# Optimization experiments

Measured on AMD Instinct MI355X. Metric: run time of the kernel, lower is better.

The kernel has to match this reference:

```python
import jax, jax.numpy as jnp
import numpy as np

B, L, E, H = 2, 2048, 1024, 16
D = E // H


def setup_inputs() -> dict:
    key = jax.random.key(0)
    ks = jax.random.split(key, 6)
    s = 1.0 / np.sqrt(E)
    return {
        "X": jax.random.normal(ks[0], (B, L, E), dtype=jnp.float32),
        "ke_bias": jax.random.normal(ks[1], (B * H, L, L), dtype=jnp.float32) * 0.05,
        "in_proj_w": jax.random.normal(ks[2], (3 * E, E), dtype=jnp.float32) * s,
        "in_proj_b": jnp.zeros((3 * E,), dtype=jnp.float32),
        "out_proj_w": jax.random.normal(ks[3], (E, E), dtype=jnp.float32) * s,
        "out_proj_b": jnp.zeros((E,), dtype=jnp.float32),
    }


def reference(X, ke_bias, in_proj_w, in_proj_b, out_proj_w, out_proj_b):
    # Packed QKV projection, matching nn.MultiheadAttention layout.
    qkv = X @ in_proj_w.T + in_proj_b  # [B, L, 3E]
    q, k, v = jnp.split(qkv, 3, axis=-1)
    # [B, L, E] -> [B, H, L, D]
    q = q.reshape(B, L, H, D).transpose(0, 2, 1, 3)
    k = k.reshape(B, L, H, D).transpose(0, 2, 1, 3)
    v = v.reshape(B, L, H, D).transpose(0, 2, 1, 3)
    scale = 1.0 / jnp.sqrt(jnp.asarray(D, dtype=q.dtype))
    scores = jnp.einsum("bhqd,bhkd->bhqk", q * scale, k)
    scores = scores + ke_bias.reshape(B, H, L, L)  # additive knowledge bias
    A = jax.nn.softmax(scores, axis=-1)
    ctx = jnp.einsum("bhqk,bhkd->bhqd", A, v)  # [B, H, L, D]
    ctx = ctx.transpose(0, 2, 1, 3).reshape(B, L, E)
    return ctx @ out_proj_w.T + out_proj_b
```

## Files before the change

### kernel.cpp

```cpp
#include <hip/hip_runtime.h>
#include <stdint.h>

typedef __attribute__((ext_vector_type(4))) float f32x4;
typedef __attribute__((ext_vector_type(8))) short bf16x8;
typedef __attribute__((ext_vector_type(4))) short bf16x4;

#define MFMA(a, b, c) __builtin_amdgcn_mfma_f32_16x16x32_bf16(a, b, c, 0, 0, 0)

__device__ __forceinline__ short f2bf(float f) {
    unsigned u = __builtin_bit_cast(unsigned, f);
    u = (u + 0x7fffu + ((u >> 16) & 1u)) >> 16;
    return (short)u;
}

__device__ __forceinline__ unsigned cvt_pk_bf16(float lo, float hi) {
    unsigned r;
    asm("v_cvt_pk_bf16_f32 %0, %1, %2" : "=v"(r) : "v"(lo), "v"(hi));
    return r;
}

__device__ __forceinline__ void g2l16(const void* g, void* l) {
    __builtin_amdgcn_global_load_lds(
        (const __attribute__((address_space(1))) unsigned*)g,
        (__attribute__((address_space(3))) unsigned*)l, 16, 0, 0);
}

union U8 { bf16x8 v; unsigned u[4]; };
union V8 { bf16x8 v; bf16x4 h[2]; };

__global__ void cvt_bf16_kernel(const float* __restrict__ src,
                                short* __restrict__ dst, int n8) {
    int i = blockIdx.x * blockDim.x + threadIdx.x;
    if (i >= n8) return;
    const f32x4* s = (const f32x4*)src;
    f32x4 a = s[2 * i], b = s[2 * i + 1];
    bf16x8 o;
    o[0] = f2bf(a[0]); o[1] = f2bf(a[1]); o[2] = f2bf(a[2]); o[3] = f2bf(a[3]);
    o[4] = f2bf(b[0]); o[5] = f2bf(b[1]); o[6] = f2bf(b[2]); o[7] = f2bf(b[3]);
    ((bf16x8*)dst)[i] = o;
}

__global__ __launch_bounds__(256, 2) void gemm_qkv_kernel(
    const short* __restrict__ A, const short* __restrict__ W,
    const float* __restrict__ bias,
    short* __restrict__ qb, short* __restrict__ kb, short* __restrict__ vtb) {
    __shared__ short As[128 * 32];
    __shared__ short Bs[128 * 32];
    __shared__ short scrS[4][16 * 24];
    const int tid = threadIdx.x;
    const int wave = tid >> 6, lane = tid & 63;
    const int al = lane >> 4, ac = lane & 15;
    const int m0 = blockIdx.x * 128;
    const int n0 = blockIdx.y * 128;
    const int wm = wave & 1, wn = wave >> 1;

    const int crow = tid >> 2, ccol = (tid & 3) * 8;
    const short* Ag0 = A + (m0 + crow) * 1024 + ccol;
    const short* Ag1 = A + (m0 + crow + 64) * 1024 + ccol;
    const short* Wg0 = W + (n0 + crow) * 1024 + ccol;
    const short* Wg1 = W + (n0 + crow + 64) * 1024 + ccol;
    short* lA0 = &As[wave * 512];
    short* lA1 = &As[2048 + wave * 512];
    short* lB0 = &Bs[wave * 512];
    short* lB1 = &Bs[2048 + wave * 512];

    f32x4 acc[4][4];
#pragma unroll
    for (int mi = 0; mi < 4; mi++)
#pragma unroll
        for (int ni = 0; ni < 4; ni++) acc[mi][ni] = (f32x4){0.f, 0.f, 0.f, 0.f};

    for (int k0 = 0; k0 < 1024; k0 += 32) {
        __syncthreads();
        g2l16(Ag0 + k0, lA0);
        g2l16(Ag1 + k0, lA1);
        g2l16(Wg0 + k0, lB0);
        g2l16(Wg1 + k0, lB1);
        __syncthreads();
        bf16x8 af[4], bfr[4];
#pragma unroll
        for (int i = 0; i < 4; i++) {
            af[i] = *(const bf16x8*)&As[(wm * 64 + i * 16 + ac) * 32 + al * 8];
            bfr[i] = *(const bf16x8*)&Bs[(wn * 64 + i * 16 + ac) * 32 + al * 8];
        }
#pragma unroll
        for (int mi = 0; mi < 4; mi++)
#pragma unroll
            for (int ni = 0; ni < 4; ni++)
                acc[mi][ni] = MFMA(af[mi], bfr[ni], acc[mi][ni]);
    }

    const int n0w = n0 + wn * 64;
    const int which = n0w >> 10;
    short* scr = scrS[wave];
    const int lr = lane >> 2;
    const int lq = lane & 3;
    const int bglob = m0 >> 11;

#pragma unroll
    for (int mi = 0; mi < 4; mi++) {
#pragma unroll
        for (int ni = 0; ni < 4; ni++) {
            const int col0 = n0w + ni * 16;
            const float bvc = bias[col0 + ac];
            if (which == 2) {
                bf16x4 pk;
#pragma unroll
                for (int r = 0; r < 4; r++) pk[r] = f2bf(acc[mi][ni][r] + bvc);
                *(bf16x4*)&scr[ac * 24 + al * 4] = pk;
                bf16x4 v4 = *(const bf16x4*)&scr[lr * 24 + lq * 4];
                const int colv = col0 + lr;
                const int e = colv & 1023;
                const int h = e >> 6, d = e & 63;
                const int row0 = m0 + wm * 64 + mi * 16 + lq * 4;
                const int l0 = row0 & 2047;
                *(bf16x4*)&vtb[(((bglob * 16 + h) * 64 + d) * 2048) + l0] = v4;
            } else {
                const float sc = (which == 0) ? 0.18033688f : 1.0f;
#pragma unroll
                for (int r = 0; r < 4; r++)
                    scr[(al * 4 + r) * 24 + ac] = f2bf((acc[mi][ni][r] + bvc) * sc);
                bf16x4 v4 = *(const bf16x4*)&scr[lr * 24 + lq * 4];
                const int col = col0 + lq * 4;
                const int e = col & 1023;
                const int h = e >> 6, d0 = e & 63;
                const int row = m0 + wm * 64 + mi * 16 + lr;
                const int l = row & 2047;
                short* dst = (which == 0) ? qb : kb;
                *(bf16x4*)&dst[(((bglob * 16 + h) * 2048 + l) * 64) + d0] = v4;
            }
        }
    }
}

#define STAGE(B_, KB_)                                                        \
  {                                                                           \
    g2l16(Kg + ((KB_) + sr0) * 64 + scs0, &Ks[B_][sw * 512]);                 \
    g2l16(Kg + ((KB_) + sr1) * 64 + scs1, &Ks[B_][2048 + sw * 512]);          \
    g2l16(Vg + sr0 * 2048 + (KB_) + scs0, &Vs[B_][sw * 512]);                 \
    g2l16(Vg + sr1 * 2048 + (KB_) + scs1, &Vs[B_][2048 + sw * 512]);          \
  }

#define ATTN_STEP(T, CURB, BC, BN)                                            \
  {                                                                           \
    const int tn_ = ((T) + 1 < 32) ? (T) + 1 : 31;                            \
    const int kn_ = tn_ * 64;                                                 \
    STAGE((CURB) ^ 1, kn_);                                                   \
    __builtin_amdgcn_sched_barrier(0);                                        \
    f32x4 s_[4];                                                              \
    __builtin_amdgcn_s_setprio(1);                                            \
    _Pragma("unroll") for (int ni = 0; ni < 4; ni++) {                        \
        const int ko_ = (ni * 16 + ac) * 64;                                  \
        const bf16x8 kf0_ = *(const bf16x8*)&Ks[CURB][ko_ + (ca_ << 3)];      \
        const bf16x8 kf1_ = *(const bf16x8*)&Ks[CURB][ko_ + ((ca_ ^ 4) << 3)];\
        s_[ni] = MFMA(kf0_, qf0, ((f32x4){0.f, 0.f, 0.f, 0.f}));              \
        s_[ni] = MFMA(kf1_, qf1, s_[ni]);                                     \
    }                                                                         \
    __builtin_amdgcn_s_setprio(0);                                            \
    V8 vf_[4][2];                                                             \
    _Pragma("unroll") for (int nd = 0; nd < 4; nd++) {                        \
        const int vo_ = (nd * 16 + ac) * 64 + inner_;                         \
        _Pragma("unroll") for (int ss = 0; ss < 2; ss++) {                    \
            vf_[nd][ss].h[0] =                                                \
                *(const bf16x4*)&Vs[CURB][vo_ + (((4 * ss + ch_) ^ rs_) << 3)]; \
            vf_[nd][ss].h[1] =                                                \
                *(const bf16x4*)&Vs[CURB][vo_ + (((4 * ss + 2 + ch_) ^ rs_) << 3)]; \
        }                                                                     \
    }                                                                         \
    float t_[16];                                                             \
    _Pragma("unroll") for (int ni = 0; ni < 4; ni++)                          \
        _Pragma("unroll") for (int r = 0; r < 4; r++)                         \
            t_[ni * 4 + r] = __builtin_fmaf(BC[ni][r], L2E, s_[ni][r]);       \
    float ma_[8];                                                             \
    _Pragma("unroll") for (int i = 0; i < 8; i++)                             \
        ma_[i] = fmaxf(t_[i], t_[8 + i]);                                     \
    float ml_ = fmaxf(fmaxf(fmaxf(ma_[0], ma_[1]), fmaxf(ma_[2], ma_[3])),    \
                      fmaxf(fmaxf(ma_[4], ma_[5]), fmaxf(ma_[6], ma_[7])));   \
    ml_ = fmaxf(ml_, __shfl_xor(ml_, 16));                                    \
    ml_ = fmaxf(ml_, __shfl_xor(ml_, 32));                                    \
    if (__any(ml_ > m_i + 8.f)) {                \
        const float mn_ = fmaxf(m_i, ml_);                                    \
        const float a_ = __builtin_exp2f(m_i - mn_);                          \
        m_i = mn_;                                                            \
        l_i *= a_;                                                            \
        _Pragma("unroll") for (int r = 0; r < 4; r++) {                       \
            const float ar_ = __shfl(a_, al20 + r);                           \
            _Pragma("unroll") for (int nd = 0; nd < 4; nd++)                  \
                o[nd][r] *= ar_;                                              \
        }                                                                     \
    }                                                                         \
    float p_[16];                                                             \
    _Pragma("unroll") for (int i = 0; i < 16; i++)                            \
        p_[i] = __builtin_exp2f(t_[i] - m_i);                                 \
    float ps0_ = 0.f, ps1_ = 0.f, ps2_ = 0.f, ps3_ = 0.f;                     \
    _Pragma("unroll") for (int r = 0; r < 4; r++) {                           \
        ps0_ += p_[r]; ps1_ += p_[4 + r];                                     \
        ps2_ += p_[8 + r]; ps3_ += p_[12 + r];                                \
    }                                                                         \
    l_i += (ps0_ + ps1_) + (ps2_ + ps3_);                                     \
    _Pragma("unroll") for (int ni = 0; ni < 4; ni++)                          \
        BN[ni] = __builtin_nontemporal_load((const f32x4*)&bp[kn_ + ni * 16]);\
    U8 pf0_, pf1_;                                                            \
    _Pragma("unroll") for (int w = 0; w < 4; w++) {                           \
        pf0_.u[w] = cvt_pk_bf16(p_[2 * w], p_[2 * w + 1]);                    \
        pf1_.u[w] = cvt_pk_bf16(p_[8 + 2 * w], p_[8 + 2 * w + 1]);            \
    }                                                                         \
    __builtin_amdgcn_s_setprio(1);                                            \
    _Pragma("unroll") for (int nd = 0; nd < 4; nd++) {                        \
        o[nd] = MFMA(pf0_.v, vf_[nd][0].v, o[nd]);                            \
        o[nd] = MFMA(pf1_.v, vf_[nd][1].v, o[nd]);                            \
    }                                                                         \
    __builtin_amdgcn_s_setprio(0);                                            \
    asm volatile("s_waitcnt vmcnt(4) lgkmcnt(0)" ::: "memory");               \
    __builtin_amdgcn_s_barrier();                                             \
    __builtin_amdgcn_sched_barrier(0);                                        \
  }

__global__ __launch_bounds__(256, 3) void attn_kernel(
    const short* __restrict__ Qb, const short* __restrict__ Kb,
    const short* __restrict__ Vtb, const float* __restrict__ bias,
    short* __restrict__ Ctx) {
    __shared__ short Ks[2][64 * 64];
    __shared__ short Vs[2][64 * 64];
    const int tid = threadIdx.x;
    const int wave = tid >> 6, lane = tid & 63;
    const int ac = lane & 15, al = lane >> 4;
    const int al20 = al * 20;
    const int bid = blockIdx.x;
    const int bh = (bid & 7) * 4 + ((bid >> 3) >> 5);
    const int q0 = ((bid >> 3) & 31) * 64 + wave * 16;
    const long long kvbase = (long long)bh * (2048 * 64);
    const float L2E = 1.44269504088896340736f;

    const int sw = wave;
    const int sr0 = sw * 8 + (lane >> 3);
    const int sr1 = 32 + sw * 8 + (lane >> 3);
    const int scs0 = ((lane & 7) ^ (sr0 & 7)) * 8;
    const int scs1 = ((lane & 7) ^ (sr1 & 7)) * 8;
    const short* Kg = Kb + kvbase;
    const short* Vg = Vtb + kvbase;

    const int rs_ = ac & 7;
    const int ca_ = al ^ rs_;
    const int ch_ = al >> 1;
    const int inner_ = (al & 1) * 4;

    const short* qp = Qb + kvbase + (q0 + ac) * 64 + al * 8;
    const bf16x8 qf0 = *(const bf16x8*)qp;
    const bf16x8 qf1 = *(const bf16x8*)(qp + 32);
    __builtin_amdgcn_sched_barrier(0);
    STAGE(0, 0);
    __builtin_amdgcn_sched_barrier(0);
    const float* bp = bias + ((long long)bh * 2048 + q0 + ac) * 2048 + al * 4;
    f32x4 bcA[4], bcB[4];
#pragma unroll
    for (int ni = 0; ni < 4; ni++)
        bcA[ni] = __builtin_nontemporal_load((const f32x4*)&bp[ni * 16]);
    asm volatile("s_waitcnt vmcnt(4)" ::: "memory");
    __builtin_amdgcn_s_barrier();
    __builtin_amdgcn_sched_barrier(0);

    float m_i = -1e30f, l_i = 0.f;
    f32x4 o[4];
#pragma unroll
    for (int i = 0; i < 4; i++) o[i] = (f32x4){0.f, 0.f, 0.f, 0.f};

#pragma unroll 1
    for (int t = 0; t < 32; t += 2) {
        ATTN_STEP(t, 0, bcA, bcB);
        ATTN_STEP(t + 1, 1, bcB, bcA);
    }

    float lt = l_i + __shfl_xor(l_i, 16);
    lt += __shfl_xor(lt, 32);
    const float inv = 1.f / lt;
    const int b_ = bh >> 4, h_ = bh & 15;
    short* cp = Ctx + (long long)(b_ * 2048 + q0) * 1024 + h_ * 64 + ac;
#pragma unroll
    for (int r = 0; r < 4; r++) {
        const float ir_ = __shfl(inv, al20 + r);
        const int row = al * 4 + r;
#pragma unroll
        for (int nd = 0; nd < 4; nd++)
            cp[(long long)row * 1024 + nd * 16] = f2bf(o[nd][r] * ir_);
    }
}

__global__ __launch_bounds__(256, 2) void gemm_out_kernel(
    const short* __restrict__ A, const short* __restrict__ W,
    const float* __restrict__ bias, float* __restrict__ out) {
    __shared__ short As[128 * 32];
    __shared__ short Bs[128 * 32];
    __shared__ float scrF[4][16 * 28];
    const int tid = threadIdx.x;
    const int wave = tid >> 6, lane = tid & 63;
    const int al = lane >> 4, ac = lane & 15;
    const int m0 = blockIdx.x * 128;
    const int n0 = blockIdx.y * 128;
    const int wm = wave & 1, wn = wave >> 1;

    const int crow = tid >> 2, ccol = (tid & 3) * 8;
    const short* Ag0 = A + (m0 + crow) * 1024 + ccol;
    const short* Ag1 = A + (m0 + crow + 64) * 1024 + ccol;
    const short* Wg0 = W + (n0 + crow) * 1024 + ccol;
    const short* Wg1 = W + (n0 + crow + 64) * 1024 + ccol;
    short* lA0 = &As[wave * 512];
    short* lA1 = &As[2048 + wave * 512];
    short* lB0 = &Bs[wave * 512];
    short* lB1 = &Bs[2048 + wave * 512];

    f32x4 acc[4][4];
#pragma unroll
    for (int mi = 0; mi < 4; mi++)
#pragma unroll
        for (int ni = 0; ni < 4; ni++) acc[mi][ni] = (f32x4){0.f, 0.f, 0.f, 0.f};

    for (int k0 = 0; k0 < 1024; k0 += 32) {
        __syncthreads();
        g2l16(Ag0 + k0, lA0);
        g2l16(Ag1 + k0, lA1);
        g2l16(Wg0 + k0, lB0);
        g2l16(Wg1 + k0, lB1);
        __syncthreads();
        bf16x8 af[4], bfr[4];
#pragma unroll
        for (int i = 0; i < 4; i++) {
            af[i] = *(const bf16x8*)&As[(wm * 64 + i * 16 + ac) * 32 + al * 8];
            bfr[i] = *(const bf16x8*)&Bs[(wn * 64 + i * 16 + ac) * 32 + al * 8];
        }
#pragma unroll
        for (int mi = 0; mi < 4; mi++)
#pragma unroll
            for (int ni = 0; ni < 4; ni++)
                acc[mi][ni] = MFMA(af[mi], bfr[ni], acc[mi][ni]);
    }

    float* scr = scrF[wave];
    const int lr = lane >> 2, lq = lane & 3;
#pragma unroll
    for (int mi = 0; mi < 4; mi++) {
#pragma unroll
        for (int ni = 0; ni < 4; ni++) {
            const int col0 = n0 + wn * 64 + ni * 16;
            const float bvc = bias[col0 + ac];
#pragma unroll
            for (int r = 0; r < 4; r++)
                scr[(al * 4 + r) * 28 + ac] = acc[mi][ni][r] + bvc;
            f32x4 v4 = *(const f32x4*)&scr[lr * 28 + lq * 4];
            const int row = m0 + wm * 64 + mi * 16 + lr;
            *(f32x4*)&out[row * 1024 + col0 + lq * 4] = v4;
        }
    }
}

extern "C" void kernel_launch(void* const* d_in, const int* in_sizes, int n_in,
                              void* d_out, int out_size, void* d_ws,
                              size_t ws_size, hipStream_t stream) {
    const float* X = (const float*)d_in[0];
    const float* keb = (const float*)d_in[1];
    const float* Wi = (const float*)d_in[2];
    const float* bi = (const float*)d_in[3];
    const float* Wo = (const float*)d_in[4];
    const float* bo = (const float*)d_in[5];
    float* out = (float*)d_out;

    char* ws = (char*)d_ws;
    short* Xb  = (short*)(ws);
    short* Wib = (short*)(ws + 8388608);
    short* Wob = (short*)(ws + 14680064);
    short* Qb  = (short*)(ws + 16777216);
    short* Kb  = (short*)(ws + 25165824);
    short* Vtb = (short*)(ws + 33554432);
    short* Ctx = (short*)(ws + 41943040);

    cvt_bf16_kernel<<<dim3(524288 / 256), 256, 0, stream>>>(X, Xb, 524288);
    cvt_bf16_kernel<<<dim3(393216 / 256), 256, 0, stream>>>(Wi, Wib, 393216);
    cvt_bf16_kernel<<<dim3(131072 / 256), 256, 0, stream>>>(Wo, Wob, 131072);
    gemm_qkv_kernel<<<dim3(32, 24), 256, 0, stream>>>(Xb, Wib, bi, Qb, Kb, Vtb);
    attn_kernel<<<dim3(1024), 256, 0, stream>>>(Qb, Kb, Vtb, keb, Ctx);
    gemm_out_kernel<<<dim3(32, 8), 256, 0, stream>>>(Ctx, Wob, bo, out);
}
```

Baseline: 806.1 us.

## Prefetch bias two tiles ahead and raise attention occupancy to four blocks

Bias rows are now prefetched two KV tiles ahead, in pairs, from a double buffer of eight vectors. This replaces the old one-tile-ahead load that was issued late in each step. The waitcnt thresholds are adjusted per step to match, and the loop is unrolled by four with a peeled tail. Launch bounds go from 3 to 4 blocks per SM for more latency hiding, and the PV MFMAs are reordered. The extra bias registers under a tighter register budget risk spills.

```diff
diff --git a/kernel.cpp b/kernel.cpp
--- a/kernel.cpp
+++ b/kernel.cpp
@@ -141,11 +141,10 @@
     g2l16(Vg + sr1 * 2048 + (KB_) + scs1, &Vs[B_][2048 + sw * 512]);          \
   }
 
-#define ATTN_STEP(T, CURB, BC, BN)                                            \
+#define ATTN_STEP(T, CURB, BCp, ISS, BDp, VMSTR)                              \
   {                                                                           \
     const int tn_ = ((T) + 1 < 32) ? (T) + 1 : 31;                            \
-    const int kn_ = tn_ * 64;                                                 \
-    STAGE((CURB) ^ 1, kn_);                                                   \
+    STAGE((CURB) ^ 1, tn_ * 64);                                              \
     __builtin_amdgcn_sched_barrier(0);                                        \
     f32x4 s_[4];                                                              \
     __builtin_amdgcn_s_setprio(1);                                            \
@@ -157,6 +156,17 @@
         s_[ni] = MFMA(kf1_, qf1, s_[ni]);                                     \
     }                                                                         \
     __builtin_amdgcn_s_setprio(0);                                            \
+    if (ISS) {                \
+        const int ka_ = (((T) + 2 < 32) ? (T) + 2 : 31) * 64;                 \
+        const int kb2_ = (((T) + 3 < 32) ? (T) + 3 : 31) * 64;                \
+        _Pragma("unroll") for (int ni = 0; ni < 4; ni++)                      \
+            (BDp)[ni] =                                                       \
+                __builtin_nontemporal_load((const f32x4*)&bp[ka_ + ni * 16]); \
+        _Pragma("unroll") for (int ni = 0; ni < 4; ni++)                      \
+            (BDp)[4 + ni] =                                                   \
+                __builtin_nontemporal_load((const f32x4*)&bp[kb2_ + ni * 16]);\
+        __builtin_amdgcn_sched_barrier(0);                                    \
+    }                                                                         \
     V8 vf_[4][2];                                                             \
     _Pragma("unroll") for (int nd = 0; nd < 4; nd++) {                        \
         const int vo_ = (nd * 16 + ac) * 64 + inner_;                         \
@@ -170,7 +180,7 @@
     float t_[16];                                                             \
     _Pragma("unroll") for (int ni = 0; ni < 4; ni++)                          \
         _Pragma("unroll") for (int r = 0; r < 4; r++)                         \
-            t_[ni * 4 + r] = __builtin_fmaf(BC[ni][r], L2E, s_[ni][r]);       \
+            t_[ni * 4 + r] = __builtin_fmaf((BCp)[ni][r], L2E, s_[ni][r]);    \
     float ma_[8];                                                             \
     _Pragma("unroll") for (int i = 0; i < 8; i++)                             \
         ma_[i] = fmaxf(t_[i], t_[8 + i]);                                     \
@@ -198,25 +208,23 @@
         ps2_ += p_[8 + r]; ps3_ += p_[12 + r];                                \
     }                                                                         \
     l_i += (ps0_ + ps1_) + (ps2_ + ps3_);                                     \
-    _Pragma("unroll") for (int ni = 0; ni < 4; ni++)                          \
-        BN[ni] = __builtin_nontemporal_load((const f32x4*)&bp[kn_ + ni * 16]);\
     U8 pf0_, pf1_;                                                            \
     _Pragma("unroll") for (int w = 0; w < 4; w++) {                           \
         pf0_.u[w] = cvt_pk_bf16(p_[2 * w], p_[2 * w + 1]);                    \
         pf1_.u[w] = cvt_pk_bf16(p_[8 + 2 * w], p_[8 + 2 * w + 1]);            \
     }                                                                         \
     __builtin_amdgcn_s_setprio(1);                                            \
-    _Pragma("unroll") for (int nd = 0; nd < 4; nd++) {                        \
+    _Pragma("unroll") for (int nd = 0; nd < 4; nd++)                          \
         o[nd] = MFMA(pf0_.v, vf_[nd][0].v, o[nd]);                            \
+    _Pragma("unroll") for (int nd = 0; nd < 4; nd++)                          \
         o[nd] = MFMA(pf1_.v, vf_[nd][1].v, o[nd]);                            \
-    }                                                                         \
     __builtin_amdgcn_s_setprio(0);                                            \
-    asm volatile("s_waitcnt vmcnt(4) lgkmcnt(0)" ::: "memory");               \
+    asm volatile("s_waitcnt vmcnt(" VMSTR ") lgkmcnt(0)" ::: "memory");       \
     __builtin_amdgcn_s_barrier();                                             \
     __builtin_amdgcn_sched_barrier(0);                                        \
   }
 
-__global__ __launch_bounds__(256, 3) void attn_kernel(
+__global__ __launch_bounds__(256, 4) void attn_kernel(
     const short* __restrict__ Qb, const short* __restrict__ Kb,
     const short* __restrict__ Vtb, const float* __restrict__ bias,
     short* __restrict__ Ctx) {
@@ -248,15 +256,17 @@
     const short* qp = Qb + kvbase + (q0 + ac) * 64 + al * 8;
     const bf16x8 qf0 = *(const bf16x8*)qp;
     const bf16x8 qf1 = *(const bf16x8*)(qp + 32);
+    const float* bp = bias + ((long long)bh * 2048 + q0 + ac) * 2048 + al * 4;
+    f32x4 bA[8], bB[8];
+#pragma unroll
+    for (int ni = 0; ni < 4; ni++) {
+        bA[ni] = __builtin_nontemporal_load((const f32x4*)&bp[ni * 16]);
+        bA[4 + ni] = __builtin_nontemporal_load((const f32x4*)&bp[64 + ni * 16]);
+    }
     __builtin_amdgcn_sched_barrier(0);
     STAGE(0, 0);
     __builtin_amdgcn_sched_barrier(0);
-    const float* bp = bias + ((long long)bh * 2048 + q0 + ac) * 2048 + al * 4;
-    f32x4 bcA[4], bcB[4];
-#pragma unroll
-    for (int ni = 0; ni < 4; ni++)
-        bcA[ni] = __builtin_nontemporal_load((const f32x4*)&bp[ni * 16]);
-    asm volatile("s_waitcnt vmcnt(4)" ::: "memory");
+    asm volatile("s_waitcnt vmcnt(0)" ::: "memory");
     __builtin_amdgcn_s_barrier();
     __builtin_amdgcn_sched_barrier(0);
 
@@ -266,10 +276,16 @@
     for (int i = 0; i < 4; i++) o[i] = (f32x4){0.f, 0.f, 0.f, 0.f};
 
 #pragma unroll 1
-    for (int t = 0; t < 32; t += 2) {
-        ATTN_STEP(t, 0, bcA, bcB);
-        ATTN_STEP(t + 1, 1, bcB, bcA);
-    }
+    for (int tt = 0; tt < 28; tt += 4) {
+        ATTN_STEP(tt + 0, 0, bA + 0, 1, bB, "8");
+        ATTN_STEP(tt + 1, 1, bA + 4, 0, bB, "0");
+        ATTN_STEP(tt + 2, 0, bB + 0, 1, bA, "8");
+        ATTN_STEP(tt + 3, 1, bB + 4, 0, bA, "0");
+    }
+    ATTN_STEP(28, 0, bA + 0, 1, bB, "8");
+    ATTN_STEP(29, 1, bA + 4, 0, bB, "0");
+    ATTN_STEP(30, 0, bB + 0, 0, bA, "0");
+    ATTN_STEP(31, 1, bB + 4, 0, bA, "0");
 
     float lt = l_i + __shfl_xor(l_i, 16);
     lt += __shfl_xor(lt, 32);
```

New measurement: 937.6 us. 16.3% more time.
